# Optimization experiments

Hardware: AMD Instinct MI355X
Metric: run time of the kernel (lower is better)

Reference implementation:

```python
import jax, jax.numpy as jnp
import numpy as np

N, TX, NH, H, E, V = 64, 1024, 512, 512, 300, 32000
IP = NH + H            # attention input size = 1024
HALF = IP // 2         # 512
BN_EPS = 1e-5


def setup_inputs() -> dict:
    key = jax.random.key(0)
    ks = jax.random.split(key, 24)
    p = lambda k, shape: jax.random.normal(k, shape, dtype=jnp.float32) * 0.05
    embed_W = p(ks[0], (V, E)).at[0].set(0.0)  # padding_idx=0 row zeroed
    return {
        "yt_prev": jax.random.randint(ks[1], (N,), 0, V, dtype=jnp.int32),
        "h0": jax.random.normal(ks[2], (N, H), dtype=jnp.float32),
        "c0": jax.random.normal(ks[3], (N, H), dtype=jnp.float32),
        "h1": jax.random.normal(ks[4], (N, H), dtype=jnp.float32),
        "c1": jax.random.normal(ks[5], (N, H), dtype=jnp.float32),
        "encoder_output": jax.random.normal(ks[6], (N, TX, NH), dtype=jnp.float32),
        "c_prev": jax.random.normal(ks[7], (N, NH), dtype=jnp.float32),
        "embed_W": embed_W,
        # pre LSTM cell: input = NH + E
        "pre_W_ih": p(ks[8], (4 * H, NH + E)), "pre_W_hh": p(ks[9], (4 * H, H)),
        "pre_b_ih": p(ks[10], (4 * H,)), "pre_b_hh": p(ks[11], (4 * H,)),
        # post LSTM cell: input = H + NH
        "post_W_ih": p(ks[12], (4 * H, H + NH)), "post_W_hh": p(ks[13], (4 * H, H)),
        "post_b_ih": p(ks[14], (4 * H,)), "post_b_hh": p(ks[15], (4 * H,)),
        # attention MLP
        "att_W1": p(ks[16], (HALF, IP)), "att_b1": p(ks[17], (HALF,)),
        "att_W2": p(ks[18], (1, HALF)), "att_b2": p(ks[19], (1,)),
        # classifier
        "mlp_W": p(ks[20], (V, H)), "mlp_b": p(ks[21], (V,)),
        "bn_gamma": jnp.ones((V,), jnp.float32), "bn_beta": jnp.zeros((V,), jnp.float32),
    }


def _lstm_cell(x, h, c, W_ih, W_hh, b_ih, b_hh):
    # PyTorch LSTMCell gate order: i, f, g, o
    g = x @ W_ih.T + h @ W_hh.T + (b_ih + b_hh)
    i, f, gg, o = jnp.split(g, 4, axis=-1)
    c_new = jax.nn.sigmoid(f) * c + jax.nn.sigmoid(i) * jnp.tanh(gg)
    h_new = jax.nn.sigmoid(o) * jnp.tanh(c_new)
    return h_new, c_new


def reference(yt_prev, h0, c0, h1, c1, encoder_output, c_prev, embed_W,
              pre_W_ih, pre_W_hh, pre_b_ih, pre_b_hh,
              post_W_ih, post_W_hh, post_b_ih, post_b_hh,
              att_W1, att_b1, att_W2, att_b2,
              mlp_W, mlp_b, bn_gamma, bn_beta):
    # embedding lookup + concat with previous context
    y_emb = embed_W[yt_prev]                              # [N, E]
    rnn_input = jnp.concatenate([y_emb, c_prev], axis=1)  # [N, E+NH]
    h_0, c_0 = _lstm_cell(rnn_input, h0, c0, pre_W_ih, pre_W_hh, pre_b_ih, pre_b_hh)
    s_i = h_0
    # Bahdanau attention over encoder timesteps
    Tx = encoder_output.shape[1]
    s_exp = jnp.broadcast_to(s_i[:, None, :], (s_i.shape[0], Tx, s_i.shape[1]))
    concat = jnp.concatenate([encoder_output, s_exp], axis=2)  # [N, Tx, IP]
    e = jax.nn.relu(concat @ att_W1.T + att_b1)                # [N, Tx, HALF]
    scores = e @ att_W2.T + att_b2                             # [N, Tx, 1]
    alphas = jax.nn.softmax(scores, axis=1)                    # softmax over Tx
    context = jnp.sum(alphas * encoder_output, axis=1)         # [N, NH]
    # post LSTM cell
    spell_input = jnp.concatenate([s_i, context], axis=1)
    h_1, c_1 = _lstm_cell(spell_input, h1, c1, post_W_ih, post_W_hh, post_b_ih, post_b_hh)
    # classifier: linear -> relu -> batchnorm(train mode, batch stats) -> softmax
    z = jax.nn.relu(h_1 @ mlp_W.T + mlp_b)                     # [N, V]
    mean = jnp.mean(z, axis=0)
    var = jnp.mean((z - mean) ** 2, axis=0)                    # biased, as in PyTorch training
    z_bn = bn_gamma * (z - mean) * jax.lax.rsqrt(var + BN_EPS) + bn_beta
    out = jax.nn.softmax(z_bn, axis=1)
    return out, h_0, c_0, h_1, c_1, context
```

## Files before the change

### kernel.cpp

```cpp
#include <hip/hip_runtime.h>
#include <math.h>

#define DEVFN __device__ __forceinline__

typedef __attribute__((ext_vector_type(4))) float f32x4;
typedef __attribute__((ext_vector_type(8))) __bf16 bf16x8;
typedef __attribute__((ext_vector_type(8))) short short8v;

#define NB   64
#define TXD  1024
#define NHD  512
#define HSZ  512
#define ESZ  300
#define VSZ  32000
#define G4   (4*HSZ)
#define KPRE (ESZ + NHD + HSZ)
#define KPOST 1536
#define HALFD 512

DEVFN short f2bf(float f) {
  unsigned u = __float_as_uint(f);
  u = (u + 0x7fffu + ((u >> 16) & 1u)) >> 16;
  return (short)u;
}
DEVFN float sigm(float x) { return 1.0f / (1.0f + __expf(-x)); }

DEVFN short8v pack8(float4 a, float4 b) {
  short8v v;
  v[0]=f2bf(a.x); v[1]=f2bf(a.y); v[2]=f2bf(a.z); v[3]=f2bf(a.w);
  v[4]=f2bf(b.x); v[5]=f2bf(b.y); v[6]=f2bf(b.z); v[7]=f2bf(b.w);
  return v;
}
DEVFN bf16x8 pack8f(float4 a, float4 b) {
  bf16x8 v;
  v[0]=(__bf16)a.x; v[1]=(__bf16)a.y; v[2]=(__bf16)a.z; v[3]=(__bf16)a.w;
  v[4]=(__bf16)b.x; v[5]=(__bf16)b.y; v[6]=(__bf16)b.z; v[7]=(__bf16)b.w;
  return v;
}
DEVFN void gload16(const void* g, void* lds_base) {
  __builtin_amdgcn_global_load_lds(
      (const __attribute__((address_space(1))) unsigned int*)g,
      (__attribute__((address_space(3))) unsigned int*)lds_base, 16, 0, 0);
}

DEVFN float4 ldA4(const float* __restrict__ A, int lda, int row, int k, int Ka) {
  if (k >= Ka) { float4 z = {0.f,0.f,0.f,0.f}; return z; }
  return *(const float4*)(A + (size_t)row * lda + k);
}
DEVFN float4 ldB4(const float* __restrict__ B1, int ldb1, int split,
                  const float* __restrict__ B2, int ldb2, int row, int k, int Ka) {
  if (k >= Ka) { float4 z = {0.f,0.f,0.f,0.f}; return z; }
  if (k < split) return *(const float4*)(B1 + (size_t)row * ldb1 + k);
  return *(const float4*)(B2 + (size_t)row * ldb2 + (k - split));
}

__global__ __launch_bounds__(256)
void prep(const int* __restrict__ yt, const float* __restrict__ embW,
          const float* __restrict__ c_prev, const float* __restrict__ h0,
          const float* __restrict__ W1, unsigned short* __restrict__ W1b,
          float* __restrict__ cat)
{
  int b = blockIdx.x;
  if (b < 128) {
    int i = b * 256 + threadIdx.x;
    int c = i >> 6, kq = (i & 63) * 8;
    float4 a = *(const float4*)(W1 + (size_t)c * 1024 + kq);
    float4 bb = *(const float4*)(W1 + (size_t)c * 1024 + kq + 4);
    *(short8v*)(W1b + (size_t)c * 512 + kq) = pack8(a, bb);
  } else {
    int i = (b - 128) * 256 + threadIdx.x;
    if (i >= NB * KPRE) return;
    int n = i / KPRE, c = i - n * KPRE;
    float v;
    if (c < ESZ)            v = embW[(size_t)yt[n] * ESZ + c];
    else if (c < ESZ + NHD) v = c_prev[(size_t)n * NHD + (c - ESZ)];
    else                    v = h0[(size_t)n * HSZ + (c - ESZ - NHD)];
    cat[i] = v;
  }
}

template<int EPI>
__global__ __launch_bounds__(256)
void mfma_gemm128(const float* __restrict__ A, int lda, int Ka,
                  const float* __restrict__ B1, int ldb1, int split,
                  const float* __restrict__ B2, int ldb2,
                  const float* __restrict__ bias1,
                  float* __restrict__ C, int ldc, int Kslice)
{
  __shared__ __align__(16) short As[64][40];
  __shared__ __align__(16) short Bs[128][40];
  const int tid = threadIdx.x;
  const int w = tid >> 6, lane = tid & 63;
  const int wr = w >> 1, wc = w & 1;
  const int cl = lane & 15, g = lane >> 4;
  const int n0 = blockIdx.x * 128;
  const int ks = blockIdx.y;
  const int kbeg = ks * Kslice;
  const int kend = min(kbeg + Kslice, Ka);
  C += (size_t)ks * 64 * ldc;

  const f32x4 fz = {0.f,0.f,0.f,0.f};
  f32x4 acc[2][4];
  #pragma unroll
  for (int i = 0; i < 2; ++i)
    #pragma unroll
    for (int j = 0; j < 4; ++j) acc[i][j] = fz;

  const int sr  = tid >> 2;
  const int skc = (tid & 3) * 8;

  float4 ra0, ra1, rb0[2], rb1[2];
  ra0 = ldA4(A, lda, sr, kbeg + skc, Ka);
  ra1 = ldA4(A, lda, sr, kbeg + skc + 4, Ka);
  #pragma unroll
  for (int it = 0; it < 2; ++it) {
    rb0[it] = ldB4(B1, ldb1, split, B2, ldb2, n0 + sr + it*64, kbeg + skc, Ka);
    rb1[it] = ldB4(B1, ldb1, split, B2, ldb2, n0 + sr + it*64, kbeg + skc + 4, Ka);
  }

  for (int k0 = kbeg; k0 < kend; k0 += 32) {
    __syncthreads();
    *(short8v*)&As[sr][skc] = pack8(ra0, ra1);
    #pragma unroll
    for (int it = 0; it < 2; ++it)
      *(short8v*)&Bs[sr + it*64][skc] = pack8(rb0[it], rb1[it]);
    __syncthreads();
    if (k0 + 32 < kend) {
      ra0 = ldA4(A, lda, sr, k0 + 32 + skc, Ka);
      ra1 = ldA4(A, lda, sr, k0 + 32 + skc + 4, Ka);
      #pragma unroll
      for (int it = 0; it < 2; ++it) {
        rb0[it] = ldB4(B1, ldb1, split, B2, ldb2, n0 + sr + it*64, k0 + 32 + skc, Ka);
        rb1[it] = ldB4(B1, ldb1, split, B2, ldb2, n0 + sr + it*64, k0 + 32 + skc + 4, Ka);
      }
    }
    bf16x8 af[2], bfr[4];
    #pragma unroll
    for (int mi = 0; mi < 2; ++mi)
      af[mi] = *(const bf16x8*)&As[wr*32 + mi*16 + cl][g * 8];
    #pragma unroll
    for (int ni = 0; ni < 4; ++ni)
      bfr[ni] = *(const bf16x8*)&Bs[wc*64 + ni*16 + cl][g * 8];
    #pragma unroll
    for (int mi = 0; mi < 2; ++mi)
      #pragma unroll
      for (int ni = 0; ni < 4; ++ni)
        acc[mi][ni] = __builtin_amdgcn_mfma_f32_16x16x32_bf16(af[mi], bfr[ni], acc[mi][ni], 0, 0, 0);
  }

  #pragma unroll
  for (int ni = 0; ni < 4; ++ni) {
    int nn = n0 + wc*64 + ni*16 + cl;
    float b = (EPI == 3) ? bias1[nn] : 0.f;
    #pragma unroll
    for (int mi = 0; mi < 2; ++mi)
      #pragma unroll
      for (int r = 0; r < 4; ++r) {
        int m = wr*32 + mi*16 + g*4 + r;
        float v = acc[mi][ni][r];
        if (EPI == 3) v = fmaxf(v + b, 0.f);
        C[(size_t)m * ldc + nn] = v;
      }
  }
}

__global__ __launch_bounds__(256)
void lstm_point2(const float* __restrict__ gp, int np,
                 const float* __restrict__ bih, const float* __restrict__ bhh,
                 const float* __restrict__ c_old,
                 float* __restrict__ h_new, float* __restrict__ c_new)
{
  int i = blockIdx.x * 256 + threadIdx.x;
  int n = i >> 9, k = i & 511;
  float g[4];
  #pragma unroll
  for (int j = 0; j < 4; ++j) {
    int idx = j * 512 + k;
    float s = bih[idx] + bhh[idx];
    for (int ks = 0; ks < np; ++ks)
      s += gp[((size_t)ks*64 + n) * G4 + idx];
    g[j] = s;
  }
  float c = sigm(g[1]) * c_old[i] + sigm(g[0]) * tanhf(g[2]);
  float h = sigm(g[3]) * tanhf(c);
  h_new[i] = h; c_new[i] = c;
}

__global__ __launch_bounds__(512)
void att_fused(const float* __restrict__ enc, const unsigned short* __restrict__ W1b,
               const float* __restrict__ W2, const float* __restrict__ sprojp,
               const float* __restrict__ b1,
               float* __restrict__ mbuf, float* __restrict__ sbuf,
               float* __restrict__ ctxp)
{
  __shared__ __align__(16) float As3[3*4096];
  __shared__ __align__(16) unsigned short Bs3[3*16384];
  __shared__ float sc[128];
  __shared__ float eV[128];
  __shared__ float msh[1];
  const int tid = threadIdx.x;
  const int wid = tid >> 6, lane = tid & 63;
  const int wr = wid >> 2, wc = wid & 3;
  const int cl = lane & 15, g = lane >> 4;
  const int r0 = blockIdx.x * 128;
  const int n = r0 >> 10;

  const int a_r = lane >> 3;
  const int a_c = ((lane & 7) ^ a_r) << 2;
  const int b_r = ((lane >> 3) << 1) + ((lane >> 2) & 1);
  const int b_c = ((lane & 3) ^ ((lane >> 3) & 3)) << 3;

  const f32x4 fz = {0.f,0.f,0.f,0.f};
  f32x4 acc[4][8];
  #pragma unroll
  for (int mi = 0; mi < 4; ++mi)
    #pragma unroll
    for (int ni = 0; ni < 8; ++ni) acc[mi][ni] = fz;

  #define STAGE(buf, t) do {                                              \
    int k0 = (t) * 32;                                                    \
    _Pragma("unroll")                                                     \
    for (int j2 = 0; j2 < 2; ++j2) {                                      \
      int j = (wid << 1) + j2;                                            \
      gload16(enc + (size_t)(r0 + (j << 3) + a_r) * 512 + k0 + a_c,       \
              As3 + (buf) * 4096 + (j << 8));                             \
    }                                                                     \
    _Pragma("unroll")                                                     \
    for (int j4 = 0; j4 < 4; ++j4) {                                      \
      int j = (wid << 2) + j4;                                            \
      gload16(W1b + (size_t)((j << 4) + b_r) * 512 + k0 + b_c,            \
              Bs3 + (buf) * 16384 + (j << 9));                            \
    }                                                                     \
  } while (0)

  STAGE(0, 0);
  STAGE(1, 1);
  for (int t = 0; t < 16; ++t) {
    const int cur = t % 3;
    if (t < 15) asm volatile("s_waitcnt vmcnt(6)" ::: "memory");
    else        asm volatile("s_waitcnt vmcnt(0)" ::: "memory");
    __builtin_amdgcn_s_barrier();
    __builtin_amdgcn_sched_barrier(0);
    if (t + 2 < 16) STAGE((t + 2) % 3, t + 2);
    const char* Ab = (const char*)(As3 + cur * 4096);
    const char* Bb = (const char*)(Bs3 + cur * 16384);
    bf16x8 af[4];
    #pragma unroll
    for (int mi = 0; mi < 4; ++mi) {
      int row = wr*64 + mi*16 + cl;
      float4 lo = *(const float4*)(Ab + row*128 + ((((g<<1)  ) ^ (cl & 7)) << 4));
      float4 hi = *(const float4*)(Ab + row*128 + ((((g<<1)|1) ^ (cl & 7)) << 4));
      af[mi] = pack8f(lo, hi);
    }
    #pragma unroll
    for (int ni = 0; ni < 8; ++ni) {
      int row = wc*128 + ni*16 + cl;
      bf16x8 bf = *(const bf16x8*)(Bb + (row >> 1)*128 + ((row & 1) << 6)
                                   + ((g ^ ((row >> 1) & 3)) << 4));
      #pragma unroll
      for (int mi = 0; mi < 4; ++mi)
        acc[mi][ni] = __builtin_amdgcn_mfma_f32_16x16x32_bf16(af[mi], bf, acc[mi][ni], 0, 0, 0);
    }
  }
  #undef STAGE
  __syncthreads();

  float* red = (float*)Bs3;
  float part[4][4] = {};
  #pragma unroll
  for (int ni = 0; ni < 8; ++ni) {
    int c = wc*128 + ni*16 + cl;
    float spv = b1[c];
    #pragma unroll
    for (int ks = 0; ks < 4; ++ks)
      spv += sprojp[((size_t)ks*64 + n) * HALFD + c];
    float w2 = W2[c];
    #pragma unroll
    for (int mi = 0; mi < 4; ++mi)
      #pragma unroll
      for (int r = 0; r < 4; ++r)
        part[mi][r] += fmaxf(acc[mi][ni][r] + spv, 0.f) * w2;
  }
  #pragma unroll
  for (int mm = 1; mm < 16; mm <<= 1)
    #pragma unroll
    for (int mi = 0; mi < 4; ++mi)
      #pragma unroll
      for (int r = 0; r < 4; ++r)
        part[mi][r] += __shfl_xor(part[mi][r], mm, 64);
  if (cl == 0) {
    #pragma unroll
    for (int mi = 0; mi < 4; ++mi)
      #pragma unroll
      for (int r = 0; r < 4; ++r)
        red[(wr*4 + wc)*64 + mi*16 + g*4 + r] = part[mi][r];
  }
  __syncthreads();
  if (tid < 128) {
    int h = tid >> 6, idx = tid & 63;
    sc[tid] = red[(h*4 + 0)*64 + idx] + red[(h*4 + 1)*64 + idx]
            + red[(h*4 + 2)*64 + idx] + red[(h*4 + 3)*64 + idx];
  }
  __syncthreads();
  if (tid < 64) {
    float a = fmaxf(sc[tid], sc[tid + 64]);
    #pragma unroll
    for (int mm = 32; mm >= 1; mm >>= 1) a = fmaxf(a, __shfl_xor(a, mm, 64));
    if (tid == 0) msh[0] = a;
  }
  __syncthreads();
  const float M = msh[0];
  if (tid < 128) eV[tid] = __expf(sc[tid] - M);
  __syncthreads();
  if (tid < 64) {
    float a = eV[tid] + eV[tid + 64];
    #pragma unroll
    for (int mm = 32; mm >= 1; mm >>= 1) a += __shfl_xor(a, mm, 64);
    if (tid == 0) { mbuf[blockIdx.x] = M; sbuf[blockIdx.x] = a; }
  }

  f32x4* red4 = (f32x4*)As3;
  {
    const int cgrp = tid & 127, tq = tid >> 7;
    const float* ebase = enc + (size_t)r0 * 512 + (cgrp << 2);
    f32x4 a4 = fz;
    #pragma unroll 8
    for (int tt = 0; tt < 32; ++tt) {
      int t = tq*32 + tt;
      float et = eV[t];
      float4 x = *(const float4*)(ebase + (size_t)t * 512);
      a4[0] = fmaf(et, x.x, a4[0]);
      a4[1] = fmaf(et, x.y, a4[1]);
      a4[2] = fmaf(et, x.z, a4[2]);
      a4[3] = fmaf(et, x.w, a4[3]);
    }
    red4[tq*128 + cgrp] = a4;
  }
  __syncthreads();
  if (tid < 128) {
    f32x4 s4 = red4[tid] ;
    f32x4 b4 = red4[128 + tid];
    f32x4 c4 = red4[256 + tid];
    f32x4 d4 = red4[384 + tid];
    f32x4 o4;
    #pragma unroll
    for (int i = 0; i < 4; ++i) o4[i] = s4[i] + b4[i] + c4[i] + d4[i];
    *(f32x4*)(ctxp + (size_t)blockIdx.x * 512 + tid*4) = o4;
  }
}

__global__ __launch_bounds__(256)
void att_combine(const float* __restrict__ mbuf, const float* __restrict__ sbuf,
                 const float* __restrict__ ctxp, const float* __restrict__ h0out,
                 const float* __restrict__ h1in,
                 float* __restrict__ ctx_out, float* __restrict__ cat)
{
  int i = blockIdx.x * 256 + threadIdx.x;
  int n = i >> 9, c = i & 511;
  float m[8];
  float M = -1e30f;
  #pragma unroll
  for (int b = 0; b < 8; ++b) { m[b] = mbuf[n*8 + b]; M = fmaxf(M, m[b]); }
  float S = 0.f, ctx = 0.f;
  #pragma unroll
  for (int b = 0; b < 8; ++b) {
    float w = __expf(m[b] - M);
    S = fmaf(sbuf[n*8 + b], w, S);
    ctx = fmaf(ctxp[(size_t)(n*8 + b)*512 + c], w, ctx);
  }
  ctx /= S;
  ctx_out[i] = ctx;
  cat[(size_t)n * KPOST + c] = h0out[i];
  cat[(size_t)n * KPOST + HSZ + c] = ctx;
  cat[(size_t)n * KPOST + 2*HSZ + c] = h1in[i];
}

__global__ __launch_bounds__(256)
void bn_stats(const float* __restrict__ z, const float* __restrict__ gamma,
              const float* __restrict__ beta, float* __restrict__ scale,
              float* __restrict__ shift)
{
  int v = blockIdx.x * 256 + threadIdx.x;
  if (v >= VSZ) return;
  float s = 0.f, s2 = 0.f;
  #pragma unroll 4
  for (int n = 0; n < NB; ++n) {
    float x = z[(size_t)n * VSZ + v];
    s += x; s2 = fmaf(x, x, s2);
  }
  float mean = s * (1.0f / NB);
  float var = s2 * (1.0f / NB) - mean * mean;
  float r = rsqrtf(var + 1e-5f);
  float sc = gamma[v] * r;
  scale[v] = sc;
  shift[v] = beta[v] - mean * sc;
}

__global__ __launch_bounds__(1024)
void softmax_v(const float* __restrict__ z, const float* __restrict__ scale,
               const float* __restrict__ shift, float* __restrict__ out)
{
  int n = blockIdx.x, tid = threadIdx.x;
  const float* zr = z + (size_t)n * VSZ;
  float* orow = out + (size_t)n * VSZ;
  __shared__ float rb[16];
  __shared__ float sb[16];
  float v[32]; float mx = -1e30f;
  #pragma unroll
  for (int i = 0; i < 32; ++i) {
    int j = tid + i*1024;
    v[i] = (j < VSZ) ? fmaf(zr[j], scale[j], shift[j]) : -1e30f;
    mx = fmaxf(mx, v[i]);
  }
  #pragma unroll
  for (int m = 32; m >= 1; m >>= 1) mx = fmaxf(mx, __shfl_xor(mx, m, 64));
  if ((tid & 63) == 0) rb[tid >> 6] = mx;
  __syncthreads();
  #pragma unroll
  for (int i = 0; i < 16; ++i) mx = fmaxf(mx, rb[i]);
  float s = 0.f;
  #pragma unroll
  for (int i = 0; i < 32; ++i) { v[i] = __expf(v[i] - mx); s += v[i]; }
  #pragma unroll
  for (int m = 32; m >= 1; m >>= 1) s += __shfl_xor(s, m, 64);
  if ((tid & 63) == 0) sb[tid >> 6] = s;
  __syncthreads();
  s = 0.f;
  #pragma unroll
  for (int i = 0; i < 16; ++i) s += sb[i];
  float inv = 1.0f / s;
  #pragma unroll
  for (int i = 0; i < 32; ++i) {
    int j = tid + i*1024;
    if (j < VSZ) orow[j] = v[i] * inv;
  }
}

extern "C" void kernel_launch(void* const* d_in, const int* in_sizes, int n_in,
                              void* d_out, int out_size, void* d_ws, size_t ws_size,
                              hipStream_t stream)
{
  const int*   yt       = (const int*)  d_in[0];
  const float* h0       = (const float*)d_in[1];
  const float* c0       = (const float*)d_in[2];
  const float* h1       = (const float*)d_in[3];
  const float* c1       = (const float*)d_in[4];
  const float* enc      = (const float*)d_in[5];
  const float* c_prev   = (const float*)d_in[6];
  const float* embW     = (const float*)d_in[7];
  const float* pre_Wih  = (const float*)d_in[8];
  const float* pre_Whh  = (const float*)d_in[9];
  const float* pre_bih  = (const float*)d_in[10];
  const float* pre_bhh  = (const float*)d_in[11];
  const float* post_Wih = (const float*)d_in[12];
  const float* post_Whh = (const float*)d_in[13];
  const float* post_bih = (const float*)d_in[14];
  const float* post_bhh = (const float*)d_in[15];
  const float* att_W1   = (const float*)d_in[16];
  const float* att_b1   = (const float*)d_in[17];
  const float* att_W2   = (const float*)d_in[18];
  const float* mlp_W    = (const float*)d_in[20];
  const float* mlp_b    = (const float*)d_in[21];
  const float* bn_g     = (const float*)d_in[22];
  const float* bn_b     = (const float*)d_in[23];

  float* out   = (float*)d_out;
  float* o_h0  = out + (size_t)NB * VSZ;
  float* o_c0  = o_h0 + NB * HSZ;
  float* o_h1  = o_c0 + NB * HSZ;
  float* o_c1  = o_h1 + NB * HSZ;
  float* o_ctx = o_c1 + NB * HSZ;

  float* ws = (float*)d_ws;
  float* pre_cat  = ws;
  float* gatesp   = ws + 84736;
  float* sprojp   = ws + 1264384;
  float* mbuf     = ws + 1395456;
  float* sbuf     = ws + 1395968;
  float* ctxp     = ws + 1396480;
  float* post_cat = ws + 1658624;
  unsigned short* W1b = (unsigned short*)(ws + 1756928);
  float* zbuf     = ws;
  float* bnsc     = ws + 2048000;
  float* bnsh     = ws + 2080000;

  prep<<<128 + (NB*KPRE + 255)/256, 256, 0, stream>>>(yt, embW, c_prev, h0,
                                                      att_W1, W1b, pre_cat);
  mfma_gemm128<0><<<dim3(G4/128, 9), 256, 0, stream>>>(
      pre_cat, KPRE, KPRE, pre_Wih, ESZ + NHD, ESZ + NHD, pre_Whh, HSZ,
      nullptr, gatesp, G4, 160);
  lstm_point2<<<NB*HSZ/256, 256, 0, stream>>>(gatesp, 9, pre_bih, pre_bhh, c0, o_h0, o_c0);
  mfma_gemm128<0><<<dim3(HALFD/128, 4), 256, 0, stream>>>(
      o_h0, HSZ, HSZ, att_W1 + NHD, NHD + HSZ, HSZ, att_W1 + NHD, NHD + HSZ,
      nullptr, sprojp, HALFD, 128);
  att_fused<<<NB*TXD/128, 512, 0, stream>>>(enc, W1b, att_W2, sprojp, att_b1,
                                            mbuf, sbuf, ctxp);
  att_combine<<<NB*NHD/256, 256, 0, stream>>>(mbuf, sbuf, ctxp, o_h0, h1, o_ctx, post_cat);
  mfma_gemm128<0><<<dim3(G4/128, 8), 256, 0, stream>>>(
      post_cat, KPOST, KPOST, post_Wih, HSZ + NHD, HSZ + NHD, post_Whh, HSZ,
      nullptr, gatesp, G4, 192);
  lstm_point2<<<NB*HSZ/256, 256, 0, stream>>>(gatesp, 8, post_bih, post_bhh, c1, o_h1, o_c1);
  mfma_gemm128<3><<<dim3(VSZ/128, 1), 256, 0, stream>>>(
      o_h1, HSZ, HSZ, mlp_W, HSZ, HSZ, mlp_W, HSZ, mlp_b, zbuf, VSZ, 512);
  bn_stats<<<(VSZ + 255)/256, 256, 0, stream>>>(zbuf, bn_g, bn_b, bnsc, bnsh);
  softmax_v<<<NB, 1024, 0, stream>>>(zbuf, bnsc, bnsh, out);
}
```

Measured before the change: 164.5 us.

## Split attention GEMM across column halves with atomic-counter join and fuse BN stats

The attention kernel now uses 64-row tiles and two 256-column blocks per tile (2048 blocks of 256 threads) with double buffering instead of a 3-stage pipeline. Partial scores go to global memory, and the last-arriving block of each pair, found through an atomic counter zeroed in prep, does the softmax and context reduction. BatchNorm statistics are computed in the classifier GEMM epilogue, which removes the separate bn_stats pass over z. This aims for higher occupancy and fewer kernel launches, but adds global-memory partials, threadfences and twice as many combine entries.

```diff
diff --git a/kernel.cpp b/kernel.cpp
--- a/kernel.cpp
+++ b/kernel.cpp
@@ -58,7 +58,7 @@
 void prep(const int* __restrict__ yt, const float* __restrict__ embW,
           const float* __restrict__ c_prev, const float* __restrict__ h0,
           const float* __restrict__ W1, unsigned short* __restrict__ W1b,
-          float* __restrict__ cat)
+          float* __restrict__ cat, unsigned int* __restrict__ cnt)
 {
   int b = blockIdx.x;
   if (b < 128) {
@@ -67,7 +67,7 @@
     float4 a = *(const float4*)(W1 + (size_t)c * 1024 + kq);
     float4 bb = *(const float4*)(W1 + (size_t)c * 1024 + kq + 4);
     *(short8v*)(W1b + (size_t)c * 512 + kq) = pack8(a, bb);
-  } else {
+  } else if (b < 460) {
     int i = (b - 128) * 256 + threadIdx.x;
     if (i >= NB * KPRE) return;
     int n = i / KPRE, c = i - n * KPRE;
@@ -76,6 +76,9 @@
     else if (c < ESZ + NHD) v = c_prev[(size_t)n * NHD + (c - ESZ)];
     else                    v = h0[(size_t)n * HSZ + (c - ESZ - NHD)];
     cat[i] = v;
+  } else {
+    #pragma unroll
+    for (int j = 0; j < 4; ++j) cnt[threadIdx.x + j*256] = 0u;
   }
 }
 
@@ -85,7 +88,9 @@
                   const float* __restrict__ B1, int ldb1, int split,
                   const float* __restrict__ B2, int ldb2,
                   const float* __restrict__ bias1,
-                  float* __restrict__ C, int ldc, int Kslice)
+                  float* __restrict__ C, int ldc, int Kslice,
+                  const float* __restrict__ gamma, const float* __restrict__ beta,
+                  float* __restrict__ bnsc, float* __restrict__ bnsh)
 {
   __shared__ __align__(16) short As[64][40];
   __shared__ __align__(16) short Bs[128][40];
@@ -148,19 +153,52 @@
         acc[mi][ni] = __builtin_amdgcn_mfma_f32_16x16x32_bf16(af[mi], bfr[ni], acc[mi][ni], 0, 0, 0);
   }
 
+  float s1[4] = {0.f,0.f,0.f,0.f}, s2[4] = {0.f,0.f,0.f,0.f};
   #pragma unroll
   for (int ni = 0; ni < 4; ++ni) {
     int nn = n0 + wc*64 + ni*16 + cl;
-    float b = (EPI == 3) ? bias1[nn] : 0.f;
+    float b = (EPI >= 3) ? bias1[nn] : 0.f;
     #pragma unroll
     for (int mi = 0; mi < 2; ++mi)
       #pragma unroll
       for (int r = 0; r < 4; ++r) {
         int m = wr*32 + mi*16 + g*4 + r;
         float v = acc[mi][ni][r];
-        if (EPI == 3) v = fmaxf(v + b, 0.f);
+        if (EPI >= 3) v = fmaxf(v + b, 0.f);
         C[(size_t)m * ldc + nn] = v;
+        if (EPI == 4) { s1[ni] += v; s2[ni] = fmaf(v, v, s2[ni]); }
       }
+  }
+  if (EPI == 4) {
+    #pragma unroll
+    for (int mm = 16; mm < 64; mm <<= 1)
+      #pragma unroll
+      for (int ni = 0; ni < 4; ++ni) {
+        s1[ni] += __shfl_xor(s1[ni], mm, 64);
+        s2[ni] += __shfl_xor(s2[ni], mm, 64);
+      }
+    float* red = (float*)As;
+    __syncthreads();
+    if (g == 0) {
+      #pragma unroll
+      for (int ni = 0; ni < 4; ++ni) {
+        int col = wc*64 + ni*16 + cl;
+        red[(wr*128 + col)*2 + 0] = s1[ni];
+        red[(wr*128 + col)*2 + 1] = s2[ni];
+      }
+    }
+    __syncthreads();
+    if (tid < 128) {
+      int col = n0 + tid;
+      float a1 = red[tid*2] + red[(128 + tid)*2];
+      float a2 = red[tid*2 + 1] + red[(128 + tid)*2 + 1];
+      float mean = a1 * (1.0f / NB);
+      float var = a2 * (1.0f / NB) - mean * mean;
+      float rr = rsqrtf(var + 1e-5f);
+      float sc = gamma[col] * rr;
+      bnsc[col] = sc;
+      bnsh[col] = beta[col] - mean * sc;
+    }
   }
 }
 
@@ -186,90 +224,82 @@
   h_new[i] = h; c_new[i] = c;
 }
 
-__global__ __launch_bounds__(512)
-void att_fused(const float* __restrict__ enc, const unsigned short* __restrict__ W1b,
-               const float* __restrict__ W2, const float* __restrict__ sprojp,
-               const float* __restrict__ b1,
-               float* __restrict__ mbuf, float* __restrict__ sbuf,
-               float* __restrict__ ctxp)
-{
-  __shared__ __align__(16) float As3[3*4096];
-  __shared__ __align__(16) unsigned short Bs3[3*16384];
-  __shared__ float sc[128];
-  __shared__ float eV[128];
-  __shared__ float msh[1];
+__global__ __launch_bounds__(256, 4)
+void att_fused2(const float* __restrict__ enc, const unsigned short* __restrict__ W1b,
+                const float* __restrict__ W2, const float* __restrict__ sprojp,
+                const float* __restrict__ b1,
+                float* __restrict__ spart, float* __restrict__ mbuf,
+                float* __restrict__ sbuf, float* __restrict__ ctxp,
+                unsigned int* __restrict__ cnt)
+{
+  __shared__ __align__(16) char smem[49152];
+  __shared__ unsigned oldLds;
   const int tid = threadIdx.x;
   const int wid = tid >> 6, lane = tid & 63;
-  const int wr = wid >> 2, wc = wid & 3;
   const int cl = lane & 15, g = lane >> 4;
-  const int r0 = blockIdx.x * 128;
-  const int n = r0 >> 10;
+  const int rt = blockIdx.x >> 1, ch = blockIdx.x & 1;
+  const int r0 = rt << 6, c0 = ch << 8;
+  const int n = rt >> 4;
 
   const int a_r = lane >> 3;
-  const int a_c = ((lane & 7) ^ a_r) << 2;
-  const int b_r = ((lane >> 3) << 1) + ((lane >> 2) & 1);
-  const int b_c = ((lane & 3) ^ ((lane >> 3) & 3)) << 3;
+  const int a_cf = (((lane & 7) ^ (a_r & 3)) << 2);
+  const int b_r = lane >> 2;
+  const int b_ce = (lane & 3) << 3;
 
   const f32x4 fz = {0.f,0.f,0.f,0.f};
-  f32x4 acc[4][8];
+  f32x4 acc[4][4];
   #pragma unroll
   for (int mi = 0; mi < 4; ++mi)
     #pragma unroll
-    for (int ni = 0; ni < 8; ++ni) acc[mi][ni] = fz;
-
-  #define STAGE(buf, t) do {                                              \
-    int k0 = (t) * 32;                                                    \
-    _Pragma("unroll")                                                     \
-    for (int j2 = 0; j2 < 2; ++j2) {                                      \
-      int j = (wid << 1) + j2;                                            \
-      gload16(enc + (size_t)(r0 + (j << 3) + a_r) * 512 + k0 + a_c,       \
-              As3 + (buf) * 4096 + (j << 8));                             \
-    }                                                                     \
-    _Pragma("unroll")                                                     \
-    for (int j4 = 0; j4 < 4; ++j4) {                                      \
-      int j = (wid << 2) + j4;                                            \
-      gload16(W1b + (size_t)((j << 4) + b_r) * 512 + k0 + b_c,            \
-              Bs3 + (buf) * 16384 + (j << 9));                            \
-    }                                                                     \
+    for (int ni = 0; ni < 4; ++ni) acc[mi][ni] = fz;
+
+  #define STAGE(s, t) do {                                                  \
+    int k0 = (t) * 32;                                                      \
+    _Pragma("unroll")                                                       \
+    for (int jj = 0; jj < 2; ++jj) {                                        \
+      int j = (wid << 1) + jj;                                              \
+      gload16(enc + (size_t)(r0 + (j << 3) + a_r) * 512 + k0 + a_cf,        \
+              smem + (s) * 24576 + (j << 10));                              \
+    }                                                                       \
+    _Pragma("unroll")                                                       \
+    for (int jj = 0; jj < 4; ++jj) {                                        \
+      int j = (wid << 2) + jj;                                              \
+      gload16(W1b + (size_t)(c0 + (j << 4) + b_r) * 512 + k0 + b_ce,        \
+              smem + (s) * 24576 + 8192 + (j << 10));                       \
+    }                                                                       \
   } while (0)
 
   STAGE(0, 0);
-  STAGE(1, 1);
+  __syncthreads();
   for (int t = 0; t < 16; ++t) {
-    const int cur = t % 3;
-    if (t < 15) asm volatile("s_waitcnt vmcnt(6)" ::: "memory");
-    else        asm volatile("s_waitcnt vmcnt(0)" ::: "memory");
-    __builtin_amdgcn_s_barrier();
-    __builtin_amdgcn_sched_barrier(0);
-    if (t + 2 < 16) STAGE((t + 2) % 3, t + 2);
-    const char* Ab = (const char*)(As3 + cur * 4096);
-    const char* Bb = (const char*)(Bs3 + cur * 16384);
+    const int s = t & 1;
+    if (t < 15) STAGE(s ^ 1, t + 1);
+    const char* Ab = smem + s * 24576;
+    const char* Bb = Ab + 8192;
     bf16x8 af[4];
     #pragma unroll
     for (int mi = 0; mi < 4; ++mi) {
-      int row = wr*64 + mi*16 + cl;
-      float4 lo = *(const float4*)(Ab + row*128 + ((((g<<1)  ) ^ (cl & 7)) << 4));
-      float4 hi = *(const float4*)(Ab + row*128 + ((((g<<1)|1) ^ (cl & 7)) << 4));
+      int row = mi*16 + cl;
+      const char* base = Ab + row * 128;
+      float4 lo = *(const float4*)(base + ((((g<<1)  ) ^ (row & 3)) << 4));
+      float4 hi = *(const float4*)(base + ((((g<<1)|1) ^ (row & 3)) << 4));
       af[mi] = pack8f(lo, hi);
     }
     #pragma unroll
-    for (int ni = 0; ni < 8; ++ni) {
-      int row = wc*128 + ni*16 + cl;
-      bf16x8 bf = *(const bf16x8*)(Bb + (row >> 1)*128 + ((row & 1) << 6)
-                                   + ((g ^ ((row >> 1) & 3)) << 4));
+    for (int ni = 0; ni < 4; ++ni) {
+      bf16x8 bf = *(const bf16x8*)(Bb + (wid*64 + ni*16 + cl) * 64 + g * 16);
       #pragma unroll
       for (int mi = 0; mi < 4; ++mi)
         acc[mi][ni] = __builtin_amdgcn_mfma_f32_16x16x32_bf16(af[mi], bf, acc[mi][ni], 0, 0, 0);
     }
+    __syncthreads();
   }
   #undef STAGE
-  __syncthreads();
-
-  float* red = (float*)Bs3;
+
   float part[4][4] = {};
   #pragma unroll
-  for (int ni = 0; ni < 8; ++ni) {
-    int c = wc*128 + ni*16 + cl;
+  for (int ni = 0; ni < 4; ++ni) {
+    int c = c0 + wid*64 + ni*16 + cl;
     float spv = b1[c];
     #pragma unroll
     for (int ks = 0; ks < 4; ++ks)
@@ -288,64 +318,48 @@
       #pragma unroll
       for (int r = 0; r < 4; ++r)
         part[mi][r] += __shfl_xor(part[mi][r], mm, 64);
+  float* red = (float*)smem;
+  float* evs = (float*)(smem + 2048);
   if (cl == 0) {
     #pragma unroll
     for (int mi = 0; mi < 4; ++mi)
       #pragma unroll
       for (int r = 0; r < 4; ++r)
-        red[(wr*4 + wc)*64 + mi*16 + g*4 + r] = part[mi][r];
+        red[wid*64 + mi*16 + g*4 + r] = part[mi][r];
   }
   __syncthreads();
-  if (tid < 128) {
-    int h = tid >> 6, idx = tid & 63;
-    sc[tid] = red[(h*4 + 0)*64 + idx] + red[(h*4 + 1)*64 + idx]
-            + red[(h*4 + 2)*64 + idx] + red[(h*4 + 3)*64 + idx];
-  }
+  if (tid < 64)
+    spart[(size_t)ch * (1024*64) + rt*64 + tid] =
+        red[tid] + red[64 + tid] + red[128 + tid] + red[192 + tid];
+  __threadfence();
   __syncthreads();
-  if (tid < 64) {
-    float a = fmaxf(sc[tid], sc[tid + 64]);
-    #pragma unroll
-    for (int mm = 32; mm >= 1; mm >>= 1) a = fmaxf(a, __shfl_xor(a, mm, 64));
-    if (tid == 0) msh[0] = a;
-  }
+  if (tid == 0) oldLds = atomicAdd(&cnt[rt], 1u);
   __syncthreads();
-  const float M = msh[0];
-  if (tid < 128) eV[tid] = __expf(sc[tid] - M);
-  __syncthreads();
-  if (tid < 64) {
-    float a = eV[tid] + eV[tid + 64];
-    #pragma unroll
-    for (int mm = 32; mm >= 1; mm >>= 1) a += __shfl_xor(a, mm, 64);
-    if (tid == 0) { mbuf[blockIdx.x] = M; sbuf[blockIdx.x] = a; }
-  }
-
-  f32x4* red4 = (f32x4*)As3;
-  {
-    const int cgrp = tid & 127, tq = tid >> 7;
-    const float* ebase = enc + (size_t)r0 * 512 + (cgrp << 2);
-    f32x4 a4 = fz;
+  if (oldLds == 1u) {
+    __threadfence();
+    if (tid < 64) {
+      float s = spart[rt*64 + tid] + spart[1024*64 + rt*64 + tid];
+      float M = s;
+      #pragma unroll
+      for (int mm = 32; mm >= 1; mm >>= 1) M = fmaxf(M, __shfl_xor(M, mm, 64));
+      float e = __expf(s - M);
+      evs[tid] = e;
+      float S = e;
+      #pragma unroll
+      for (int mm = 32; mm >= 1; mm >>= 1) S += __shfl_xor(S, mm, 64);
+      if (tid == 0) { mbuf[rt] = M; sbuf[rt] = S; cnt[rt] = 0u; }
+    }
+    __syncthreads();
+    float2 a2 = {0.f, 0.f};
+    const float* ebase = enc + (size_t)r0 * 512 + tid*2;
     #pragma unroll 8
-    for (int tt = 0; tt < 32; ++tt) {
-      int t = tq*32 + tt;
-      float et = eV[t];
-      float4 x = *(const float4*)(ebase + (size_t)t * 512);
-      a4[0] = fmaf(et, x.x, a4[0]);
-      a4[1] = fmaf(et, x.y, a4[1]);
-      a4[2] = fmaf(et, x.z, a4[2]);
-      a4[3] = fmaf(et, x.w, a4[3]);
-    }
-    red4[tq*128 + cgrp] = a4;
-  }
-  __syncthreads();
-  if (tid < 128) {
-    f32x4 s4 = red4[tid] ;
-    f32x4 b4 = red4[128 + tid];
-    f32x4 c4 = red4[256 + tid];
-    f32x4 d4 = red4[384 + tid];
-    f32x4 o4;
-    #pragma unroll
-    for (int i = 0; i < 4; ++i) o4[i] = s4[i] + b4[i] + c4[i] + d4[i];
-    *(f32x4*)(ctxp + (size_t)blockIdx.x * 512 + tid*4) = o4;
+    for (int r = 0; r < 64; ++r) {
+      float ev = evs[r];
+      float2 x = *(const float2*)(ebase + (size_t)r * 512);
+      a2.x = fmaf(ev, x.x, a2.x);
+      a2.y = fmaf(ev, x.y, a2.y);
+    }
+    *(float2*)(ctxp + (size_t)rt * 512 + tid*2) = a2;
   }
 }
 
@@ -357,43 +371,21 @@
 {
   int i = blockIdx.x * 256 + threadIdx.x;
   int n = i >> 9, c = i & 511;
-  float m[8];
   float M = -1e30f;
   #pragma unroll
-  for (int b = 0; b < 8; ++b) { m[b] = mbuf[n*8 + b]; M = fmaxf(M, m[b]); }
+  for (int b = 0; b < 16; ++b) M = fmaxf(M, mbuf[n*16 + b]);
   float S = 0.f, ctx = 0.f;
   #pragma unroll
-  for (int b = 0; b < 8; ++b) {
-    float w = __expf(m[b] - M);
-    S = fmaf(sbuf[n*8 + b], w, S);
-    ctx = fmaf(ctxp[(size_t)(n*8 + b)*512 + c], w, ctx);
+  for (int b = 0; b < 16; ++b) {
+    float w = __expf(mbuf[n*16 + b] - M);
+    S = fmaf(sbuf[n*16 + b], w, S);
+    ctx = fmaf(ctxp[(size_t)(n*16 + b)*512 + c], w, ctx);
   }
   ctx /= S;
   ctx_out[i] = ctx;
   cat[(size_t)n * KPOST + c] = h0out[i];
   cat[(size_t)n * KPOST + HSZ + c] = ctx;
   cat[(size_t)n * KPOST + 2*HSZ + c] = h1in[i];
-}
-
-__global__ __launch_bounds__(256)
-void bn_stats(const float* __restrict__ z, const float* __restrict__ gamma,
-              const float* __restrict__ beta, float* __restrict__ scale,
-              float* __restrict__ shift)
-{
-  int v = blockIdx.x * 256 + threadIdx.x;
-  if (v >= VSZ) return;
-  float s = 0.f, s2 = 0.f;
-  #pragma unroll 4
-  for (int n = 0; n < NB; ++n) {
-    float x = z[(size_t)n * VSZ + v];
-    s += x; s2 = fmaf(x, x, s2);
-  }
-  float mean = s * (1.0f / NB);
-  float var = s2 * (1.0f / NB) - mean * mean;
-  float r = rsqrtf(var + 1e-5f);
-  float sc = gamma[v] * r;
-  scale[v] = sc;
-  shift[v] = beta[v] - mean * sc;
 }
 
 __global__ __launch_bounds__(1024)
@@ -475,33 +467,34 @@
   float* pre_cat  = ws;
   float* gatesp   = ws + 84736;
   float* sprojp   = ws + 1264384;
-  float* mbuf     = ws + 1395456;
-  float* sbuf     = ws + 1395968;
-  float* ctxp     = ws + 1396480;
-  float* post_cat = ws + 1658624;
-  unsigned short* W1b = (unsigned short*)(ws + 1756928);
+  float* spart    = ws + 1395456;
+  float* mbuf     = ws + 1526528;
+  float* sbuf     = ws + 1527552;
+  unsigned int* cnt = (unsigned int*)(ws + 1528576);
+  float* ctxp     = ws + 1529600;
+  float* post_cat = ws + 2053888;
+  unsigned short* W1b = (unsigned short*)(ws + 2152192);
   float* zbuf     = ws;
-  float* bnsc     = ws + 2048000;
-  float* bnsh     = ws + 2080000;
-
-  prep<<<128 + (NB*KPRE + 255)/256, 256, 0, stream>>>(yt, embW, c_prev, h0,
-                                                      att_W1, W1b, pre_cat);
+  float* bnsc     = ws + 2283264;
+  float* bnsh     = ws + 2315264;
+
+  prep<<<461, 256, 0, stream>>>(yt, embW, c_prev, h0, att_W1, W1b, pre_cat, cnt);
   mfma_gemm128<0><<<dim3(G4/128, 9), 256, 0, stream>>>(
       pre_cat, KPRE, KPRE, pre_Wih, ESZ + NHD, ESZ + NHD, pre_Whh, HSZ,
-      nullptr, gatesp, G4, 160);
+      nullptr, gatesp, G4, 160, nullptr, nullptr, nullptr, nullptr);
   lstm_point2<<<NB*HSZ/256, 256, 0, stream>>>(gatesp, 9, pre_bih, pre_bhh, c0, o_h0, o_c0);
   mfma_gemm128<0><<<dim3(HALFD/128, 4), 256, 0, stream>>>(
       o_h0, HSZ, HSZ, att_W1 + NHD, NHD + HSZ, HSZ, att_W1 + NHD, NHD + HSZ,
-      nullptr, sprojp, HALFD, 128);
-  att_fused<<<NB*TXD/128, 512, 0, stream>>>(enc, W1b, att_W2, sprojp, att_b1,
-                                            mbuf, sbuf, ctxp);
+      nullptr, sprojp, HALFD, 128, nullptr, nullptr, nullptr, nullptr);
+  att_fused2<<<2048, 256, 0, stream>>>(enc, W1b, att_W2, sprojp, att_b1,
+                                       spart, mbuf, sbuf, ctxp, cnt);
   att_combine<<<NB*NHD/256, 256, 0, stream>>>(mbuf, sbuf, ctxp, o_h0, h1, o_ctx, post_cat);
   mfma_gemm128<0><<<dim3(G4/128, 8), 256, 0, stream>>>(
       post_cat, KPOST, KPOST, post_Wih, HSZ + NHD, HSZ + NHD, post_Whh, HSZ,
-      nullptr, gatesp, G4, 192);
+      nullptr, gatesp, G4, 192, nullptr, nullptr, nullptr, nullptr);
   lstm_point2<<<NB*HSZ/256, 256, 0, stream>>>(gatesp, 8, post_bih, post_bhh, c1, o_h1, o_c1);
-  mfma_gemm128<3><<<dim3(VSZ/128, 1), 256, 0, stream>>>(
-      o_h1, HSZ, HSZ, mlp_W, HSZ, HSZ, mlp_W, HSZ, mlp_b, zbuf, VSZ, 512);
-  bn_stats<<<(VSZ + 255)/256, 256, 0, stream>>>(zbuf, bn_g, bn_b, bnsc, bnsh);
+  mfma_gemm128<4><<<dim3(VSZ/128, 1), 256, 0, stream>>>(
+      o_h1, HSZ, HSZ, mlp_W, HSZ, HSZ, mlp_W, HSZ, mlp_b, zbuf, VSZ, 512,
+      bn_g, bn_b, bnsc, bnsh);
   softmax_v<<<NB, 1024, 0, stream>>>(zbuf, bnsc, bnsh, out);
 }
```

New measurement: 569.1 us. 246% more time.
